# Performance work log

Measured on AMD Instinct MI355X. Metric: run time of the kernel, lower is better.

Reference implementation:

```python
import jax, jax.numpy as jnp
import numpy as np


def setup_inputs() -> dict:
    key = jax.random.key(0)
    kx, ky = jax.random.split(key)
    B, N, C, G = 16, 8192, 64, 512
    x = jax.random.normal(kx, (B, N, C), dtype=jnp.float32)
    y = jax.random.randint(ky, (B, N), 0, G).astype(jnp.int64)
    return {"x": x, "y": y, "g": G}


def reference(x, y, g):
    # x: [B, N, C], y: [B, N] group ids (y < 0 -> dropped via sentinel class g)
    N = x.shape[1]
    y = jnp.where(y < 0, g, y)
    # one_hot over g+1 classes, drop the sentinel column -> [B, N, G]
    oh = jax.nn.one_hot(y, g + 1, dtype=x.dtype)[..., :g]
    # (x[:, :, None, :] * oh[..., None]).mean(1)  ==  einsum / N
    feature = jnp.einsum('bng,bnc->bgc', oh, x) / N  # [B, G, C]
    mask = oh.sum(axis=1) > 0                        # [B, G]
    return feature, mask
```

## Files before the change

kernel.cpp:

```cpp
#include <hip/hip_runtime.h>


#define B_ 16
#define N_ 8192
#define C_ 64
#define G_ 512
#define CHUNK 1024
#define NCHUNK (N_ / CHUNK)
#define CAP 272

__global__ __launch_bounds__(256, 8)
void gap_gather3(const float* __restrict__ x, const int* __restrict__ y,
                 float* __restrict__ feature, float* __restrict__ maskout) {
    const int tid  = threadIdx.x;
    const int lane = tid & 63;
    const int wave = tid >> 6;
    const int blk  = blockIdx.x;
    const int b    = blk >> 7;
    const int g    = ((blk & 127) << 2) + wave;

    const int*   yb = y + b * N_;
    const float* xb = x + (size_t)b * (size_t)(N_ * C_);

    __shared__ int sy[CHUNK];
    __shared__ int widx[4][CAP];

    float a0 = 0, a1 = 0, a2 = 0, a3 = 0, a4 = 0, a5 = 0, a6 = 0, a7 = 0;
    int cnt = 0;
    int tot = 0;

    int4 pre = *reinterpret_cast<const int4*>(yb + tid * 4);

    for (int ch = 0; ch < NCHUNK; ++ch) {
        __syncthreads();
        *reinterpret_cast<int4*>(&sy[tid * 4]) = pre;
        __syncthreads();
        if (ch + 1 < NCHUNK)
            pre = *reinterpret_cast<const int4*>(yb + (ch + 1) * CHUNK + tid * 4);

        const int nbase = ch * CHUNK;
        for (int sub = 0; sub < CHUNK / 256; ++sub) {
            const int4 yv = *reinterpret_cast<const int4*>(&sy[sub * 256 + lane * 4]);
            const int nl = nbase + sub * 256 + lane * 4;

            #define COMPACT(VAL, OFF) do {                                        \
                unsigned long long m = __ballot((VAL) == g);                      \
                int p = __builtin_amdgcn_mbcnt_hi((unsigned)(m >> 32),            \
                        __builtin_amdgcn_mbcnt_lo((unsigned)m, 0));               \
                if ((VAL) == g) widx[wave][cnt + p] = nl + (OFF);                 \
                int pc = (int)__popcll(m);                                        \
                cnt += pc; tot += pc;                                             \
            } while (0)
            COMPACT(yv.x, 0);
            COMPACT(yv.y, 1);
            COMPACT(yv.z, 2);
            COMPACT(yv.w, 3);
            #undef COMPACT

            int fo = 0;
            while (cnt - fo >= 8) {
                const int4 ia = *reinterpret_cast<const int4*>(&widx[wave][fo]);
                const int4 ib = *reinterpret_cast<const int4*>(&widx[wave][fo + 4]);
                a0 += xb[(size_t)ia.x * C_ + lane];
                a1 += xb[(size_t)ia.y * C_ + lane];
                a2 += xb[(size_t)ia.z * C_ + lane];
                a3 += xb[(size_t)ia.w * C_ + lane];
                a4 += xb[(size_t)ib.x * C_ + lane];
                a5 += xb[(size_t)ib.y * C_ + lane];
                a6 += xb[(size_t)ib.z * C_ + lane];
                a7 += xb[(size_t)ib.w * C_ + lane];
                fo += 8;
            }
            const int rem = cnt - fo;
            if (fo > 0 && rem > 0) {
                int t = (lane < rem) ? widx[wave][fo + lane] : 0;
                if (lane < rem) widx[wave][lane] = t;
            }
            cnt = rem;
        }
    }

    for (int i = 0; i < cnt; ++i)
        a0 += xb[(size_t)widx[wave][i] * C_ + lane];

    const float acc = ((a0 + a1) + (a2 + a3)) + ((a4 + a5) + (a6 + a7));
    feature[((size_t)b * G_ + g) * C_ + lane] = acc * (1.0f / (float)N_);
    if (lane == 0) maskout[b * G_ + g] = (tot > 0) ? 1.0f : 0.0f;
}

extern "C" void kernel_launch(void* const* d_in, const int* in_sizes, int n_in,
                              void* d_out, int out_size, void* d_ws, size_t ws_size,
                              hipStream_t stream) {
    const float* x = (const float*)d_in[0];
    const int*   y = (const int*)d_in[1];
    float* feature = (float*)d_out;
    float* maskout = (float*)d_out + (size_t)B_ * G_ * C_;

    const int grid = B_ * (G_ / 4);
    gap_gather3<<<grid, 256, 0, stream>>>(x, y, feature, maskout);
}
```

Measured before the change: 91.37 us.

## Collect all group indices first, then batch-gather rows at the end

Each wave now walks the ballot mask bit by bit and appends matching row indices to a per-wave LDS list, capped at 96 entries. Rows beyond the cap are gathered immediately. Rows in the list are no longer gathered as soon as eight accumulate; all of them are gathered after the scan in an unrolled loop that keeps eight loads in flight. This removes the per-sub-block compaction and shift of leftover indices, and turns scattered small gathers into one batched gather phase with more memory parallelism. The costs are a serial per-bit scalar loop in the scan, a single-lane LDS write, and a later start for the global loads.

Result: faster. 83.63 us (-8.5%).

```diff
diff --git a/kernel.cpp b/kernel.cpp
--- a/kernel.cpp
+++ b/kernel.cpp
@@ -7,11 +7,11 @@
 #define G_ 512
 #define CHUNK 1024
 #define NCHUNK (N_ / CHUNK)
-#define CAP 272
+#define CAP 96
 
 __global__ __launch_bounds__(256, 8)
-void gap_gather3(const float* __restrict__ x, const int* __restrict__ y,
-                 float* __restrict__ feature, float* __restrict__ maskout) {
+void gap_v5(const float* __restrict__ x, const int* __restrict__ y,
+            float* __restrict__ feature, float* __restrict__ maskout) {
     const int tid  = threadIdx.x;
     const int lane = tid & 63;
     const int wave = tid >> 6;
@@ -27,7 +27,6 @@
 
     float a0 = 0, a1 = 0, a2 = 0, a3 = 0, a4 = 0, a5 = 0, a6 = 0, a7 = 0;
     int cnt = 0;
-    int tot = 0;
 
     int4 pre = *reinterpret_cast<const int4*>(yb + tid * 4);
 
@@ -39,53 +38,50 @@
             pre = *reinterpret_cast<const int4*>(yb + (ch + 1) * CHUNK + tid * 4);
 
         const int nbase = ch * CHUNK;
+        #pragma unroll
         for (int sub = 0; sub < CHUNK / 256; ++sub) {
             const int4 yv = *reinterpret_cast<const int4*>(&sy[sub * 256 + lane * 4]);
-            const int nl = nbase + sub * 256 + lane * 4;
-
-            #define COMPACT(VAL, OFF) do {                                        \
-                unsigned long long m = __ballot((VAL) == g);                      \
-                int p = __builtin_amdgcn_mbcnt_hi((unsigned)(m >> 32),            \
-                        __builtin_amdgcn_mbcnt_lo((unsigned)m, 0));               \
-                if ((VAL) == g) widx[wave][cnt + p] = nl + (OFF);                 \
-                int pc = (int)__popcll(m);                                        \
-                cnt += pc; tot += pc;                                             \
+            const int base = nbase + sub * 256;
+            #define COLLECT(VAL, OFF) do {                                    \
+                unsigned long long m = __ballot((VAL) == g);                  \
+                while (m) {  \
+                    const int l = __builtin_ctzll(m); m &= m - 1;             \
+                    const int idx = base + l * 4 + (OFF);                     \
+                    if (cnt < CAP) {                                          \
+                        if (lane == 0) widx[wave][cnt] = idx;                 \
+                        ++cnt;                                                \
+                    } else {        \
+                        a0 += xb[(size_t)idx * C_ + lane];                    \
+                    }                                                         \
+                }                                                             \
             } while (0)
-            COMPACT(yv.x, 0);
-            COMPACT(yv.y, 1);
-            COMPACT(yv.z, 2);
-            COMPACT(yv.w, 3);
-            #undef COMPACT
-
-            int fo = 0;
-            while (cnt - fo >= 8) {
-                const int4 ia = *reinterpret_cast<const int4*>(&widx[wave][fo]);
-                const int4 ib = *reinterpret_cast<const int4*>(&widx[wave][fo + 4]);
-                a0 += xb[(size_t)ia.x * C_ + lane];
-                a1 += xb[(size_t)ia.y * C_ + lane];
-                a2 += xb[(size_t)ia.z * C_ + lane];
-                a3 += xb[(size_t)ia.w * C_ + lane];
-                a4 += xb[(size_t)ib.x * C_ + lane];
-                a5 += xb[(size_t)ib.y * C_ + lane];
-                a6 += xb[(size_t)ib.z * C_ + lane];
-                a7 += xb[(size_t)ib.w * C_ + lane];
-                fo += 8;
-            }
-            const int rem = cnt - fo;
-            if (fo > 0 && rem > 0) {
-                int t = (lane < rem) ? widx[wave][fo + lane] : 0;
-                if (lane < rem) widx[wave][lane] = t;
-            }
-            cnt = rem;
+            COLLECT(yv.x, 0);
+            COLLECT(yv.y, 1);
+            COLLECT(yv.z, 2);
+            COLLECT(yv.w, 3);
+            #undef COLLECT
         }
     }
 
-    for (int i = 0; i < cnt; ++i)
+    int i = 0;
+    for (; i + 8 <= cnt; i += 8) {
+        const int4 ia = *reinterpret_cast<const int4*>(&widx[wave][i]);
+        const int4 ib = *reinterpret_cast<const int4*>(&widx[wave][i + 4]);
+        a0 += xb[(size_t)ia.x * C_ + lane];
+        a1 += xb[(size_t)ia.y * C_ + lane];
+        a2 += xb[(size_t)ia.z * C_ + lane];
+        a3 += xb[(size_t)ia.w * C_ + lane];
+        a4 += xb[(size_t)ib.x * C_ + lane];
+        a5 += xb[(size_t)ib.y * C_ + lane];
+        a6 += xb[(size_t)ib.z * C_ + lane];
+        a7 += xb[(size_t)ib.w * C_ + lane];
+    }
+    for (; i < cnt; ++i)
         a0 += xb[(size_t)widx[wave][i] * C_ + lane];
 
     const float acc = ((a0 + a1) + (a2 + a3)) + ((a4 + a5) + (a6 + a7));
     feature[((size_t)b * G_ + g) * C_ + lane] = acc * (1.0f / (float)N_);
-    if (lane == 0) maskout[b * G_ + g] = (tot > 0) ? 1.0f : 0.0f;
+    if (lane == 0) maskout[b * G_ + g] = (cnt > 0) ? 1.0f : 0.0f;
 }
 
 extern "C" void kernel_launch(void* const* d_in, const int* in_sizes, int n_in,
@@ -94,8 +90,8 @@
     const float* x = (const float*)d_in[0];
     const int*   y = (const int*)d_in[1];
     float* feature = (float*)d_out;
-    float* maskout = (float*)d_out + (size_t)B_ * G_ * C_;
+    float* maskout = feature + (size_t)B_ * G_ * C_;
 
     const int grid = B_ * (G_ / 4);
-    gap_gather3<<<grid, 256, 0, stream>>>(x, y, feature, maskout);
+    gap_v5<<<grid, 256, 0, stream>>>(x, y, feature, maskout);
 }
```
